# Optimization experiments

Hardware: AMD Instinct MI355X
Metric: run time of the kernel (lower is better)

## Reference

```python
import jax, jax.numpy as jnp
import numpy as np

B = 32768      # batch of graphs
H = 128        # hidden_channels
L = 3          # num message-passing layers
T = 3          # num_timesteps
NB, NJ = 1, 12 # base nodes, joint nodes
NN = NB + NJ   # 13 nodes per graph
OBS_W = 47     # obs features per timestep
BASE_IDX = np.array(list(range(9)) + [45, 46])   # 11 base features per timestep
JOINT_IDX = np.array(list(range(9, 45)))          # 36 joint features per timestep
BASE_F = T * len(BASE_IDX)                        # 33
JOINT_F = (len(JOINT_IDX) // NJ) * T              # 9

# fixed tree edges, both directions (24 edges per graph)
_n2n = np.array([[0, 0, 0, 0, 1, 2, 4, 5, 7, 8, 10, 11],
                 [1, 4, 7, 10, 2, 3, 5, 6, 8, 9, 11, 12]])
SRC = np.concatenate([_n2n[0], _n2n[1]])
DST = np.concatenate([_n2n[1], _n2n[0]])


def setup_inputs() -> dict:
    key = jax.random.key(0)
    ks = jax.random.split(key, 10)
    s = 0.05
    return {
        "obs": jax.random.normal(ks[0], (B, T * OBS_W), dtype=jnp.float32),
        "We_b": jax.random.normal(ks[1], (H, BASE_F), dtype=jnp.float32) * s,
        "be_b": jax.random.normal(ks[2], (H,), dtype=jnp.float32) * s,
        "We_j": jax.random.normal(ks[3], (H, JOINT_F), dtype=jnp.float32) * s,
        "be_j": jax.random.normal(ks[4], (H,), dtype=jnp.float32) * s,
        "W_rel": jax.random.normal(ks[5], (L, H, H), dtype=jnp.float32) * s,
        "W_root": jax.random.normal(ks[6], (L, H, H), dtype=jnp.float32) * s,
        "b_rel": jax.random.normal(ks[7], (L, H), dtype=jnp.float32) * s,
        "W_dec": jax.random.normal(ks[8], (1, H), dtype=jnp.float32) * s,
        "b_dec": jax.random.normal(ks[9], (1,), dtype=jnp.float32) * s,
        "src": jnp.asarray(SRC, dtype=jnp.int32),
        "dst": jnp.asarray(DST, dtype=jnp.int32),
    }


def reference(obs, We_b, be_b, We_j, be_j, W_rel, W_root, b_rel, W_dec, b_dec, src, dst):
    b = obs.shape[0]
    elu = jax.nn.elu
    # ---- obs -> per-node features ----
    obs3 = obs[:, :T * OBS_W].reshape(b, T, OBS_W)
    base_feat = obs3[:, :, BASE_IDX].reshape(b, NB, BASE_F)                 # [B,1,33]
    joint_feat = (obs3[:, :, JOINT_IDX]
                  .reshape(b, T, len(JOINT_IDX) // NJ, NJ)
                  .transpose(0, 3, 1, 2)
                  .reshape(b, NJ, JOINT_F))                                  # [B,12,9]
    # ---- encoders ----
    xb = elu(jnp.einsum('bnf,hf->bnh', base_feat, We_b) + be_b)
    xj = elu(jnp.einsum('bnf,hf->bnh', joint_feat, We_j) + be_j)
    x = jnp.concatenate([xb, xj], axis=1)                                    # [B,13,H]
    # ---- GraphConv layers: out = W_root x + W_rel (scatter_add of x_src at dst) + b ----
    for l in range(L):
        agg = jnp.zeros_like(x).at[:, dst].add(x[:, src])                    # [B,13,H]
        x = elu(jnp.einsum('bnh,oh->bno', agg, W_rel[l]) + b_rel[l]
                + jnp.einsum('bnh,oh->bno', x, W_root[l]))
    # ---- per-joint decoder ----
    out = jnp.einsum('bnh,oh->bno', x[:, NB:], W_dec) + b_dec                # [B,12,1]
    return out.reshape(b, NJ)
```

## Files before the change

### kernel.cpp

```cpp
#include <hip/hip_runtime.h>

#define H      128
#define OBSROW 141
#define GPB    16
#define NT     512

typedef __bf16 bf16x8 __attribute__((ext_vector_type(8)));
typedef float  f32x4  __attribute__((ext_vector_type(4)));

__device__ __forceinline__ float eluf(float v) {
    return v > 0.0f ? v : (__expf(v) - 1.0f);
}
__device__ __forceinline__ f32x4 mf(bf16x8 a, bf16x8 b, f32x4 c) {
    return __builtin_amdgcn_mfma_f32_16x16x32_bf16(a, b, c, 0, 0, 0);
}

#define WS_ROOT 49152
#define WS_EB   98304
#define WS_EJ   106496
#define WS_TOT  110592

__global__ void convert_weights(const float* __restrict__ Wr, const float* __restrict__ Wo,
                                const float* __restrict__ Web, const float* __restrict__ Wej,
                                __bf16* __restrict__ ws) {
    const int i = blockIdx.x * 256 + threadIdx.x;
    if (i < WS_ROOT) {
        ws[i] = (__bf16)Wr[i];
    } else if (i < WS_EB) {
        ws[i] = (__bf16)Wo[i - WS_ROOT];
    } else if (i < WS_EJ) {
        const int j = i - WS_EB, o = j >> 6, f = j & 63;
        ws[i] = (__bf16)(f < 33 ? Web[o*33 + f] : 0.0f);
    } else if (i < WS_TOT) {
        const int j = i - WS_EJ, o = j >> 5, f = j & 31;
        ws[i] = (__bf16)(f < 9 ? Wej[o*9 + f] : 0.0f);
    }
}

#define XIDX(n,hc,g,hi) (((((n)*16 + (hc))*16 + (g))*8) + (hi))

__launch_bounds__(NT, 4)
__global__ void gnn_fused(const float* __restrict__ obs,
                          const float* __restrict__ be_b, const float* __restrict__ be_j,
                          const float* __restrict__ b_rel,
                          const float* __restrict__ W_dec, const float* __restrict__ b_dec,
                          const __bf16* __restrict__ wsb,
                          float* __restrict__ out, int B)
{
    __shared__ __align__(16) unsigned short Xs[13*2048];
    __shared__ __align__(16) unsigned short Fs[7168];

    const int tid  = threadIdx.x;
    const int wave = tid >> 6;
    const int lane = tid & 63;
    const int q    = lane >> 4;
    const int c    = lane & 15;
    const int g0   = blockIdx.x * GPB;
    const int jt   = wave;
    const int o    = jt*16 + c;

    static constexpr int ODEG[13]    = {4,2,2,1,2,2,1,2,2,1,2,2,1};
    static constexpr int ODST[13][4] = {
        {1,4,7,10},{0,2,0,0},{1,3,0,0},{2,0,0,0},{0,5,0,0},{4,6,0,0},{5,0,0,0},
        {0,8,0,0},{7,9,0,0},{8,0,0,0},{0,11,0,0},{10,12,0,0},{11,0,0,0}};

    {
        float* raw = (float*)Xs;
        for (int i = tid; i < GPB*OBSROW; i += NT) {
            const int g = i / OBSROW, col = i - g*OBSROW;
            raw[i] = ((g0 + g) < B) ? obs[(g0+g)*OBSROW + col] : 0.0f;
            (void)col;
        }
    }
    __syncthreads();

    {
        const float* raw = (const float*)Xs;
        for (int s = tid; s < 6144; s += NT) {
            const int jj = s >> 9, rem = s & 511;
            const int fc = rem >> 7, g = (rem >> 3) & 15, hi = rem & 7;
            const int f = fc*8 + hi;
            float v = 0.0f;
            if (f < 9)
                v = raw[g*OBSROW + (f/3)*47 + 9 + (f%3)*12 + jj];
            *(__bf16*)&Fs[s] = (__bf16)v;
        }
        for (int s = tid; s < 1024; s += NT) {
            const int fc = s >> 7, rem = s & 127, g = rem >> 3, hi = rem & 7;
            const int f = fc*8 + hi;
            float v = 0.0f;
            if (f < 33) {
                const int tt = f / 11, i2 = f % 11;
                v = raw[g*OBSROW + tt*47 + (i2 < 9 ? i2 : 36 + i2)];
            }
            *(__bf16*)&Fs[6144 + s] = (__bf16)v;
        }
    }
    __syncthreads();

    {
        const bf16x8 u0 = *(const bf16x8*)(wsb + WS_EB + o*64 + q*8);
        const bf16x8 u1 = *(const bf16x8*)(wsb + WS_EB + o*64 + 32 + q*8);
        const bf16x8 a0 = *(const bf16x8*)&Fs[6144 + q*128 + c*8];
        const bf16x8 a1 = *(const bf16x8*)&Fs[6144 + 512 + q*128 + c*8];
        const float bias = be_b[o];
        f32x4 acc = {bias, bias, bias, bias};
        acc = mf(a0, u0, acc);
        acc = mf(a1, u1, acc);
        #pragma unroll
        for (int r = 0; r < 4; r++)
            *(__bf16*)&Xs[XIDX(0, jt*2 + (c>>3), q*4 + r, c & 7)] = (__bf16)eluf(acc[r]);
    }
    {
        const bf16x8 uj = *(const bf16x8*)(wsb + WS_EJ + o*32 + q*8);
        const float bias = be_j[o];
        #pragma unroll
        for (int jj = 0; jj < 12; jj++) {
            const bf16x8 a = *(const bf16x8*)&Fs[jj*512 + q*128 + c*8];
            f32x4 acc = {bias, bias, bias, bias};
            acc = mf(a, uj, acc);
            #pragma unroll
            for (int r = 0; r < 4; r++)
                *(__bf16*)&Xs[XIDX(1+jj, jt*2 + (c>>3), q*4 + r, c & 7)] = (__bf16)eluf(acc[r]);
        }
    }
    __syncthreads();

    const unsigned short* xr = Xs + q*128 + c*8;
    #pragma unroll 1
    for (int l = 0; l < 3; l++) {
        const __bf16* wr = wsb + l*16384 + o*128 + q*8;
        const __bf16* wo = wsb + WS_ROOT + l*16384 + o*128 + q*8;
        const float bias = b_rel[l*H + o];

        f32x4 acc[13];
        #pragma unroll
        for (int n = 0; n < 13; n++) acc[n] = (f32x4){bias, bias, bias, bias};

        #pragma unroll 1
        for (int h = 0; h < 2; h++) {
            const bf16x8 br0 = *(const bf16x8*)(wr + (2*h+0)*32);
            const bf16x8 br1 = *(const bf16x8*)(wr + (2*h+1)*32);
            const bf16x8 bo0 = *(const bf16x8*)(wo + (2*h+0)*32);
            const bf16x8 bo1 = *(const bf16x8*)(wo + (2*h+1)*32);
            const unsigned short* xh = xr + 2*h*512;
            #pragma unroll
            for (int n = 0; n < 13; n++) {
                const bf16x8 xa0 = *(const bf16x8*)(xh + n*2048);
                const bf16x8 xa1 = *(const bf16x8*)(xh + n*2048 + 512);
                acc[n] = mf(xa0, bo0, acc[n]);
                acc[n] = mf(xa1, bo1, acc[n]);
                f32x4 y = {0.f,0.f,0.f,0.f};
                y = mf(xa0, br0, y);
                y = mf(xa1, br1, y);
                #pragma unroll
                for (int e = 0; e < 4; e++)
                    if (e < ODEG[n]) acc[ODST[n][e]] += y;
            }
        }
        __syncthreads();
        {
            const int hc = jt*2 + (c >> 3);
            const int hi = c & 7;
            #pragma unroll
            for (int n = 0; n < 13; n++) {
                #pragma unroll
                for (int r = 0; r < 4; r++)
                    *(__bf16*)&Xs[XIDX(n, hc, q*4 + r, hi)] = (__bf16)eluf(acc[n][r]);
            }
        }
        __syncthreads();
    }

    {
        const unsigned short* xdec = Xs + q*512 + c*8;
        float wd[32];
        #pragma unroll
        for (int i4 = 0; i4 < 8; i4++) {
            const float4 wv = *(const float4*)&W_dec[q*32 + i4*4];
            wd[i4*4+0] = wv.x; wd[i4*4+1] = wv.y; wd[i4*4+2] = wv.z; wd[i4*4+3] = wv.w;
        }
        const float bd = b_dec[0];
        for (int j = wave; j < 12; j += 8) {
            float s = 0.0f;
            #pragma unroll
            for (int hq = 0; hq < 4; hq++) {
                const bf16x8 xv = *(const bf16x8*)(xdec + (j+1)*2048 + hq*128);
                #pragma unroll
                for (int hi2 = 0; hi2 < 8; hi2++)
                    s += (float)xv[hi2] * wd[hq*8 + hi2];
            }
            s += __shfl_xor(s, 16);
            s += __shfl_xor(s, 32);
            if (q == 0 && (g0 + c) < B)
                out[(g0 + c)*12 + j] = s + bd;
        }
    }
}

extern "C" void kernel_launch(void* const* d_in, const int* in_sizes, int n_in,
                              void* d_out, int out_size, void* d_ws, size_t ws_size,
                              hipStream_t stream) {
    const float* obs   = (const float*)d_in[0];
    const float* We_b  = (const float*)d_in[1];
    const float* be_b  = (const float*)d_in[2];
    const float* We_j  = (const float*)d_in[3];
    const float* be_j  = (const float*)d_in[4];
    const float* W_rel = (const float*)d_in[5];
    const float* W_root= (const float*)d_in[6];
    const float* b_rel = (const float*)d_in[7];
    const float* W_dec = (const float*)d_in[8];
    const float* b_dec = (const float*)d_in[9];
    float* out = (float*)d_out;
    __bf16* wsb = (__bf16*)d_ws;

    const int B = in_sizes[0] / OBSROW;
    convert_weights<<<(WS_TOT + 255) / 256, 256, 0, stream>>>(W_rel, W_root, We_b, We_j, wsb);
    const int blocks = (B + GPB - 1) / GPB;
    gnn_fused<<<blocks, NT, 0, stream>>>(obs, be_b, be_j, b_rel, W_dec, b_dec,
                                         wsb, out, B);
}
```

Measured before the change: 200.2 us.

## Halve waves per block, give each wave 32 outputs with swapped MFMA operands

Drops the block from 8 to 4 waves. Each wave now computes 32 output channels, holding all W_rel and W_root fragments for its rows in registers, so each node's activation fragments loaded from LDS are reused across two output tiles. It also swaps the MFMA operand order (weights as A, activations as B), which lets each lane write four consecutive bf16 outputs as one packed 64-bit LDS store instead of four scalar stores. In exchange register pressure rises (26 accumulators plus 16 weight vectors) and occupancy per block drops, with launch bounds lowered to match.

Result: slower. 208.5 us (+4.2%).

```diff
diff --git a/kernel.cpp b/kernel.cpp
--- a/kernel.cpp
+++ b/kernel.cpp
@@ -3,7 +3,7 @@
 #define H      128
 #define OBSROW 141
 #define GPB    16
-#define NT     512
+#define NT     256
 
 typedef __bf16 bf16x8 __attribute__((ext_vector_type(8)));
 typedef float  f32x4  __attribute__((ext_vector_type(4)));
@@ -13,6 +13,15 @@
 }
 __device__ __forceinline__ f32x4 mf(bf16x8 a, bf16x8 b, f32x4 c) {
     return __builtin_amdgcn_mfma_f32_16x16x32_bf16(a, b, c, 0, 0, 0);
+}
+__device__ __forceinline__ void store_pk4(unsigned short* dst, f32x4 a) {
+    union { unsigned short u[4]; unsigned long long v; } pk;
+    #pragma unroll
+    for (int r = 0; r < 4; r++) {
+        __bf16 b = (__bf16)eluf(a[r]);
+        pk.u[r] = *(unsigned short*)&b;
+    }
+    *(unsigned long long*)dst = pk.v;
 }
 
 #define WS_ROOT 49152
@@ -39,7 +48,7 @@
 
 #define XIDX(n,hc,g,hi) (((((n)*16 + (hc))*16 + (g))*8) + (hi))
 
-__launch_bounds__(NT, 4)
+__launch_bounds__(NT, 2)
 __global__ void gnn_fused(const float* __restrict__ obs,
                           const float* __restrict__ be_b, const float* __restrict__ be_j,
                           const float* __restrict__ b_rel,
@@ -56,20 +65,20 @@
     const int q    = lane >> 4;
     const int c    = lane & 15;
     const int g0   = blockIdx.x * GPB;
-    const int jt   = wave;
-    const int o    = jt*16 + c;
 
     static constexpr int ODEG[13]    = {4,2,2,1,2,2,1,2,2,1,2,2,1};
     static constexpr int ODST[13][4] = {
         {1,4,7,10},{0,2,0,0},{1,3,0,0},{2,0,0,0},{0,5,0,0},{4,6,0,0},{5,0,0,0},
         {0,8,0,0},{7,9,0,0},{8,0,0,0},{0,11,0,0},{10,12,0,0},{11,0,0,0}};
 
+    const int hcs0 = wave*4 + (q>>1);
+    const int wofs = c*8 + (q&1)*4;
+
     {
         float* raw = (float*)Xs;
         for (int i = tid; i < GPB*OBSROW; i += NT) {
-            const int g = i / OBSROW, col = i - g*OBSROW;
-            raw[i] = ((g0 + g) < B) ? obs[(g0+g)*OBSROW + col] : 0.0f;
-            (void)col;
+            const int g = i / OBSROW;
+            raw[i] = ((g0 + g) < B) ? obs[(g0+g)*OBSROW + (i - g*OBSROW)] : 0.0f;
         }
     }
     __syncthreads();
@@ -99,75 +108,84 @@
     __syncthreads();
 
     {
-        const bf16x8 u0 = *(const bf16x8*)(wsb + WS_EB + o*64 + q*8);
-        const bf16x8 u1 = *(const bf16x8*)(wsb + WS_EB + o*64 + 32 + q*8);
+        const int orow = wave*32 + c;
         const bf16x8 a0 = *(const bf16x8*)&Fs[6144 + q*128 + c*8];
         const bf16x8 a1 = *(const bf16x8*)&Fs[6144 + 512 + q*128 + c*8];
-        const float bias = be_b[o];
-        f32x4 acc = {bias, bias, bias, bias};
-        acc = mf(a0, u0, acc);
-        acc = mf(a1, u1, acc);
-        #pragma unroll
-        for (int r = 0; r < 4; r++)
-            *(__bf16*)&Xs[XIDX(0, jt*2 + (c>>3), q*4 + r, c & 7)] = (__bf16)eluf(acc[r]);
-    }
-    {
-        const bf16x8 uj = *(const bf16x8*)(wsb + WS_EJ + o*32 + q*8);
-        const float bias = be_j[o];
-        #pragma unroll
-        for (int jj = 0; jj < 12; jj++) {
-            const bf16x8 a = *(const bf16x8*)&Fs[jj*512 + q*128 + c*8];
-            f32x4 acc = {bias, bias, bias, bias};
-            acc = mf(a, uj, acc);
-            #pragma unroll
-            for (int r = 0; r < 4; r++)
-                *(__bf16*)&Xs[XIDX(1+jj, jt*2 + (c>>3), q*4 + r, c & 7)] = (__bf16)eluf(acc[r]);
+        #pragma unroll
+        for (int s = 0; s < 2; s++) {
+            const bf16x8 u0 = *(const bf16x8*)(wsb + WS_EB + (orow + s*16)*64 + q*8);
+            const bf16x8 u1 = *(const bf16x8*)(wsb + WS_EB + (orow + s*16)*64 + 32 + q*8);
+            const float4 b4 = *(const float4*)&be_b[wave*32 + s*16 + q*4];
+            f32x4 acc = {b4.x, b4.y, b4.z, b4.w};
+            acc = mf(u0, a0, acc);
+            acc = mf(u1, a1, acc);
+            store_pk4(&Xs[(hcs0 + s*2)*128 + wofs], acc);
+        }
+        #pragma unroll
+        for (int s = 0; s < 2; s++) {
+            const bf16x8 uj = *(const bf16x8*)(wsb + WS_EJ + (orow + s*16)*32 + q*8);
+            const float4 b4 = *(const float4*)&be_j[wave*32 + s*16 + q*4];
+            const f32x4 bias = {b4.x, b4.y, b4.z, b4.w};
+            #pragma unroll
+            for (int jj = 0; jj < 12; jj++) {
+                const bf16x8 a = *(const bf16x8*)&Fs[jj*512 + q*128 + c*8];
+                f32x4 acc = bias;
+                acc = mf(uj, a, acc);
+                store_pk4(&Xs[(1+jj)*2048 + (hcs0 + s*2)*128 + wofs], acc);
+            }
         }
     }
     __syncthreads();
 
-    const unsigned short* xr = Xs + q*128 + c*8;
+    const unsigned short* xb_base = Xs + q*128 + c*8;
     #pragma unroll 1
     for (int l = 0; l < 3; l++) {
-        const __bf16* wr = wsb + l*16384 + o*128 + q*8;
-        const __bf16* wo = wsb + WS_ROOT + l*16384 + o*128 + q*8;
-        const float bias = b_rel[l*H + o];
-
-        f32x4 acc[13];
-        #pragma unroll
-        for (int n = 0; n < 13; n++) acc[n] = (f32x4){bias, bias, bias, bias};
-
-        #pragma unroll 1
-        for (int h = 0; h < 2; h++) {
-            const bf16x8 br0 = *(const bf16x8*)(wr + (2*h+0)*32);
-            const bf16x8 br1 = *(const bf16x8*)(wr + (2*h+1)*32);
-            const bf16x8 bo0 = *(const bf16x8*)(wo + (2*h+0)*32);
-            const bf16x8 bo1 = *(const bf16x8*)(wo + (2*h+1)*32);
-            const unsigned short* xh = xr + 2*h*512;
-            #pragma unroll
-            for (int n = 0; n < 13; n++) {
-                const bf16x8 xa0 = *(const bf16x8*)(xh + n*2048);
-                const bf16x8 xa1 = *(const bf16x8*)(xh + n*2048 + 512);
-                acc[n] = mf(xa0, bo0, acc[n]);
-                acc[n] = mf(xa1, bo1, acc[n]);
-                f32x4 y = {0.f,0.f,0.f,0.f};
-                y = mf(xa0, br0, y);
-                y = mf(xa1, br1, y);
-                #pragma unroll
-                for (int e = 0; e < 4; e++)
-                    if (e < ODEG[n]) acc[ODST[n][e]] += y;
-            }
+        const __bf16* wr = wsb + l*16384;
+        const __bf16* wo = wsb + WS_ROOT + l*16384;
+        bf16x8 Wr[2][4], Wt[2][4];
+        #pragma unroll
+        for (int s = 0; s < 2; s++) {
+            const int row = (wave*32 + s*16 + c)*128 + q*8;
+            #pragma unroll
+            for (int ks = 0; ks < 4; ks++) {
+                Wr[s][ks] = *(const bf16x8*)(wr + row + ks*32);
+                Wt[s][ks] = *(const bf16x8*)(wo + row + ks*32);
+            }
+        }
+        f32x4 acc[13][2];
+        #pragma unroll
+        for (int s = 0; s < 2; s++) {
+            const float4 b4 = *(const float4*)&b_rel[l*H + wave*32 + s*16 + q*4];
+            const f32x4 bias = {b4.x, b4.y, b4.z, b4.w};
+            #pragma unroll
+            for (int n = 0; n < 13; n++) acc[n][s] = bias;
+        }
+        #pragma unroll
+        for (int n = 0; n < 13; n++) {
+            bf16x8 xb[4];
+            #pragma unroll
+            for (int ks = 0; ks < 4; ks++)
+                xb[ks] = *(const bf16x8*)(xb_base + n*2048 + ks*512);
+            f32x4 y0 = {0.f,0.f,0.f,0.f}, y1 = {0.f,0.f,0.f,0.f};
+            #pragma unroll
+            for (int ks = 0; ks < 4; ks++) {
+                acc[n][0] = mf(Wt[0][ks], xb[ks], acc[n][0]);
+                acc[n][1] = mf(Wt[1][ks], xb[ks], acc[n][1]);
+                y0 = mf(Wr[0][ks], xb[ks], y0);
+                y1 = mf(Wr[1][ks], xb[ks], y1);
+            }
+            #pragma unroll
+            for (int e = 0; e < 4; e++)
+                if (e < ODEG[n]) {
+                    acc[ODST[n][e]][0] += y0;
+                    acc[ODST[n][e]][1] += y1;
+                }
         }
         __syncthreads();
-        {
-            const int hc = jt*2 + (c >> 3);
-            const int hi = c & 7;
-            #pragma unroll
-            for (int n = 0; n < 13; n++) {
-                #pragma unroll
-                for (int r = 0; r < 4; r++)
-                    *(__bf16*)&Xs[XIDX(n, hc, q*4 + r, hi)] = (__bf16)eluf(acc[n][r]);
-            }
+        #pragma unroll
+        for (int n = 0; n < 13; n++) {
+            store_pk4(&Xs[n*2048 +  hcs0     *128 + wofs], acc[n][0]);
+            store_pk4(&Xs[n*2048 + (hcs0 + 2)*128 + wofs], acc[n][1]);
         }
         __syncthreads();
     }
@@ -181,7 +199,7 @@
             wd[i4*4+0] = wv.x; wd[i4*4+1] = wv.y; wd[i4*4+2] = wv.z; wd[i4*4+3] = wv.w;
         }
         const float bd = b_dec[0];
-        for (int j = wave; j < 12; j += 8) {
+        for (int j = wave; j < 12; j += 4) {
             float s = 0.0f;
             #pragma unroll
             for (int hq = 0; hq < 4; hq++) {
```
